# Optimization experiments

Hardware: AMD Instinct MI355X
Metric: run time of the kernel (lower is better)

## Reference

```python
import jax, jax.numpy as jnp
import numpy as np

H = 16  # n_heads
D = 64  # d_keys


def setup_inputs() -> dict:
    key = jax.random.key(0)
    ks = jax.random.split(key, 11)
    b, n, dm = 2, 2048, 1024
    s = 1.0 / np.sqrt(dm)
    return {
        "q": jax.random.normal(ks[0], (b, n, dm), jnp.float32),
        "k": jax.random.normal(ks[1], (b, n, dm), jnp.float32),
        "v": jax.random.normal(ks[2], (b, n, dm), jnp.float32),
        "Wq": jax.random.normal(ks[3], (dm, H * D), jnp.float32) * s,
        "bq": jax.random.normal(ks[4], (H * D,), jnp.float32) * 0.01,
        "Wk": jax.random.normal(ks[5], (dm, H * D), jnp.float32) * s,
        "bk": jax.random.normal(ks[6], (H * D,), jnp.float32) * 0.01,
        "Wv": jax.random.normal(ks[7], (dm, H * D), jnp.float32) * s,
        "bv": jax.random.normal(ks[8], (H * D,), jnp.float32) * 0.01,
        "Wo": jax.random.normal(ks[9], (H * D, dm), jnp.float32) * s,
        "bo": jax.random.normal(ks[10], (dm,), jnp.float32) * 0.01,
    }


def reference(q, k, v, Wq, bq, Wk, bk, Wv, bv, Wo, bo):
    b, n_q, _ = q.shape
    n_k = k.shape[1]
    # projections -> [b, n, h, d]
    qh = (q @ Wq + bq).reshape(b, n_q, H, D)
    kh = (k @ Wk + bk).reshape(b, n_k, H, D)
    vh = (v @ Wv + bv).reshape(b, n_k, H, D)
    # scores [b, h, n, m]
    scores = jnp.einsum('bnhd,bmhd->bhnm', qh, kh)
    causal = jnp.triu(jnp.ones((n_q, n_k), dtype=bool), k=1)  # True above diag
    scores = jnp.where(causal, -jnp.inf, scores)
    att = jax.nn.softmax(scores / np.sqrt(D).astype(np.float32), axis=-1)
    att_out = jnp.einsum('bhnm,bmhd->bnhd', att, vh).reshape(b, n_q, H * D)
    return att_out @ Wo + bo
```

## Files before the change

### kernel.cpp

```cpp
#include <hip/hip_runtime.h>

typedef float f32x4 __attribute__((ext_vector_type(4)));
typedef __bf16 bf16x8 __attribute__((ext_vector_type(8)));
typedef __bf16 bf16x4 __attribute__((ext_vector_type(4)));
typedef __bf16 bf16_t;

#define NH 16
#define DH 64
#define SEQ 2048
#define DM 1024

extern "C" hipError_t hipMemPtrGetInfo(void* ptr, size_t* size);

__device__ __forceinline__ bf16x8 ld8(const bf16_t* p) { return *(const bf16x8*)p; }
__device__ __forceinline__ void st8(bf16_t* p, bf16x8 v) { *(bf16x8*)p = v; }

__device__ __forceinline__ void gl_lds16(const bf16_t* g, bf16_t* l)
{
    __builtin_amdgcn_global_load_lds(
        (const __attribute__((address_space(1))) unsigned int*)g,
        (__attribute__((address_space(3))) unsigned int*)l, 16, 0, 0);
}

__global__ __launch_bounds__(256) void fill_sentinel(float* out, unsigned n, float val)
{
    unsigned stride = gridDim.x * blockDim.x;
    for (unsigned i = blockIdx.x * blockDim.x + threadIdx.x; i < n; i += stride)
        out[i] = val;
}

__global__ __launch_bounds__(256) void prep(
    const float* __restrict__ q, const float* __restrict__ k,
    const float* __restrict__ v,
    const float* __restrict__ w0, const float* __restrict__ w1,
    const float* __restrict__ w2, const float* __restrict__ w3,
    bf16_t* __restrict__ xb, bf16_t* __restrict__ wt)
{
    int z = blockIdx.z;
    if (z < 3) {
        const float* src = (z == 0) ? q : (z == 1) ? k : v;
        bf16_t* dst = xb + (size_t)z * (4096u * 1024u);
        size_t i8 = ((size_t)blockIdx.x * 256 + threadIdx.x) * 8;
        f32x4 u = *(const f32x4*)(src + i8);
        f32x4 w = *(const f32x4*)(src + i8 + 4);
        bf16x8 h = { (bf16_t)u.x, (bf16_t)u.y, (bf16_t)u.z, (bf16_t)u.w,
                     (bf16_t)w.x, (bf16_t)w.y, (bf16_t)w.z, (bf16_t)w.w };
        st8(dst + i8, h);
    } else {
        int x = blockIdx.x;
        if (x >= 1024) return;
        int w = x >> 8, rem = x & 255;
        int bx = rem & 15, by = rem >> 4;
        const float* in = (w == 0) ? w0 : (w == 1) ? w1 : (w == 2) ? w2 : w3;
        bf16_t* out = wt + (size_t)w * DM * DM;
        __shared__ __align__(16) bf16_t tile[64][72];
        int t = threadIdx.x;
        int k0 = by * 64, n0 = bx * 64;
        int r0 = t >> 4, c0 = (t & 15) * 4;
        for (int p = 0; p < 4; p++) {
            int r = r0 + p * 16;
            const float* src = in + (size_t)(k0 + r) * DM + n0 + c0;
            for (int i = 0; i < 4; i++) tile[r][c0 + i] = (bf16_t)src[i];
        }
        __syncthreads();
        for (int p = 0; p < 4; p++) {
            int rn = r0 + p * 16;
            bf16_t* dst = out + (size_t)(n0 + rn) * DM + k0 + c0;
            for (int i = 0; i < 4; i++) dst[i] = tile[c0 + i][rn];
        }
    }
}

__device__ __forceinline__ void gemm_epilogue(
    f32x4 (&acc)[4][4], const float* bias, bf16_t* out, float* outf,
    int mode, int out_is_f32, int m0, int n0, int wr0, int wc0, int g, int l16)
{
    float scale = (mode == 0) ? 0.125f : 1.0f;
    for (int mi = 0; mi < 4; mi++) {
        int mbase = m0 + wr0 + mi * 16 + g * 4;
        for (int ni = 0; ni < 4; ni++) {
            int col = n0 + wc0 + ni * 16 + l16;
            float bv = bias[col];
            if (mode == 2) {
                int bb = mbase >> 11, nn0 = mbase & 2047;
                int h = col >> 6, d = col & 63;
                bf16x4 pv;
                for (int r = 0; r < 4; r++) pv[r] = (bf16_t)(acc[mi][ni][r] + bv);
                *(bf16x4*)(out + ((size_t)(bb * NH + h) * DH + d) * SEQ + nn0) = pv;
            } else {
                for (int r = 0; r < 4; r++) {
                    int mr = mbase + r;
                    float sv = (acc[mi][ni][r] + bv) * scale;
                    if (mode == 3) {
                        if (out_is_f32) outf[(size_t)mr * 1024 + col] = sv;
                        else            out[(size_t)mr * 1024 + col] = (bf16_t)sv;
                    } else {
                        int bb = mr >> 11, nn = mr & 2047;
                        int h = col >> 6, d = col & 63;
                        out[((size_t)(bb * NH + h) * SEQ + nn) * DH + d] = (bf16_t)sv;
                    }
                }
            }
        }
    }
}

__global__ __launch_bounds__(256) void gemm_fast(
    const bf16_t* __restrict__ xb_base, const bf16_t* __restrict__ wt_base,
    const float* __restrict__ b0, const float* __restrict__ b1,
    const float* __restrict__ b2, bf16_t* __restrict__ out_base,
    float* __restrict__ outf, int mode_base, int out_is_f32)
{
    int z = blockIdx.z;
    const bf16_t* X    = xb_base + (size_t)z * (4096u * 1024u);
    const bf16_t* WT   = wt_base + (size_t)z * DM * DM;
    const float* bias  = (z == 0) ? b0 : (z == 1) ? b1 : b2;
    bf16_t* out = out_base + (size_t)z * (4096u * 1024u);
    int mode = mode_base + z;

    int m0 = blockIdx.x * 128;
    int n0 = blockIdx.y * 128;

    __shared__ __align__(16) bf16_t Alds[128 * 64];
    __shared__ __align__(16) bf16_t Blds[128 * 64];

    int t = threadIdx.x;
    int lane = t & 63, wave = t >> 6;
    int g = lane >> 4, l16 = lane & 15;
    int wr0 = (wave >> 1) * 64, wc0 = (wave & 1) * 64;
    int crow = lane >> 3;
    int ccol = (lane & 7) * 8;

    f32x4 acc[4][4] = {};

    for (int k0 = 0; k0 < DM; k0 += 64) {
        __syncthreads();
        for (int c = wave; c < 16; c += 4) {
            int row = c * 8 + crow;
            gl_lds16(X  + (size_t)(m0 + row) * DM + k0 + ccol,
                     Alds + c * 512 + lane * 8);
            gl_lds16(WT + (size_t)(n0 + row) * DM + k0 + ccol,
                     Blds + c * 512 + lane * 8);
        }
        __syncthreads();
        for (int kk = 0; kk < 2; kk++) {
            bf16x8 af[4], bfr[4];
            for (int i = 0; i < 4; i++)
                af[i] = ld8(Alds + (wr0 + i * 16 + l16) * 64 + kk * 32 + g * 8);
            for (int i = 0; i < 4; i++)
                bfr[i] = ld8(Blds + (wc0 + i * 16 + l16) * 64 + kk * 32 + g * 8);
            for (int mi = 0; mi < 4; mi++)
                for (int ni = 0; ni < 4; ni++)
                    acc[mi][ni] = __builtin_amdgcn_mfma_f32_16x16x32_bf16(
                        af[mi], bfr[ni], acc[mi][ni], 0, 0, 0);
        }
    }
    gemm_epilogue(acc, bias, out, outf, mode, out_is_f32, m0, n0, wr0, wc0, g, l16);
}

__global__ __launch_bounds__(256) void gemm_mha(
    const float* __restrict__ x0, const float* __restrict__ x1,
    const float* __restrict__ x2, const bf16_t* __restrict__ xb,
    const bf16_t* __restrict__ wt_base,
    const float* __restrict__ b0, const float* __restrict__ b1,
    const float* __restrict__ b2, bf16_t* __restrict__ out_base,
    float* __restrict__ outf, int mode_base, int out_is_f32)
{
    int z = blockIdx.z;
    const float* Xf    = (z == 0) ? x0 : (z == 1) ? x1 : x2;
    const bf16_t* WT   = wt_base + (size_t)z * DM * DM;
    const float* bias  = (z == 0) ? b0 : (z == 1) ? b1 : b2;
    bf16_t* out = out_base + (size_t)z * (4096u * 1024u);
    int mode = mode_base + z;

    int m0 = blockIdx.x * 128;
    int n0 = blockIdx.y * 128;

    __shared__ __align__(16) bf16_t Alds[128 * 64];
    __shared__ __align__(16) bf16_t Blds[128 * 64];

    int t = threadIdx.x;
    int lane = t & 63, wave = t >> 6;
    int g = lane >> 4, l16 = lane & 15;
    int wr0 = (wave >> 1) * 64, wc0 = (wave & 1) * 64;

    f32x4 acc[4][4] = {};
    int srow = t >> 3, sk = (t & 7) * 8;

    for (int k0 = 0; k0 < DM; k0 += 64) {
        __syncthreads();
        if (mode < 3) {
            for (int p = 0; p < 4; p++) {
                int r = srow + p * 32;
                const float* s4 = Xf + (size_t)(m0 + r) * DM + k0 + sk;
                f32x4 u = *(const f32x4*)s4;
                f32x4 w = *(const f32x4*)(s4 + 4);
                bf16x8 h = { (bf16_t)u.x, (bf16_t)u.y, (bf16_t)u.z, (bf16_t)u.w,
                             (bf16_t)w.x, (bf16_t)w.y, (bf16_t)w.z, (bf16_t)w.w };
                st8(Alds + r * 64 + sk, h);
            }
        } else {
            for (int p = 0; p < 4; p++) {
                int r = srow + p * 32;
                st8(Alds + r * 64 + sk, ld8(xb + (size_t)(m0 + r) * DM + k0 + sk));
            }
        }
        for (int p = 0; p < 4; p++) {
            int r = srow + p * 32;
            st8(Blds + r * 64 + sk, ld8(WT + (size_t)(n0 + r) * DM + k0 + sk));
        }
        __syncthreads();
        for (int kk = 0; kk < 2; kk++) {
            bf16x8 af[4], bfr[4];
            for (int i = 0; i < 4; i++)
                af[i] = ld8(Alds + (wr0 + i * 16 + l16) * 64 + kk * 32 + g * 8);
            for (int i = 0; i < 4; i++)
                bfr[i] = ld8(Blds + (wc0 + i * 16 + l16) * 64 + kk * 32 + g * 8);
            for (int mi = 0; mi < 4; mi++)
                for (int ni = 0; ni < 4; ni++)
                    acc[mi][ni] = __builtin_amdgcn_mfma_f32_16x16x32_bf16(
                        af[mi], bfr[ni], acc[mi][ni], 0, 0, 0);
        }
    }
    gemm_epilogue(acc, bias, out, outf, mode, out_is_f32, m0, n0, wr0, wc0, g, l16);
}

__global__ __launch_bounds__(512) void attn(
    const bf16_t* __restrict__ Qh, const bf16_t* __restrict__ Kh,
    const bf16_t* __restrict__ VT, bf16_t* __restrict__ att)
{
    int bhx = blockIdx.x;
    int yy  = blockIdx.y;
    int p   = (yy < 8) ? yy : 23 - yy;
    int TB  = 2 * p + 2;

    const bf16_t* Qb = Qh + (size_t)bhx * SEQ * DH;
    const bf16_t* Kb = Kh + (size_t)bhx * SEQ * DH;
    const bf16_t* Vb = VT + (size_t)bhx * DH * SEQ;

    __shared__ __align__(16) bf16_t Klds[2][64 * 72];
    __shared__ __align__(16) bf16_t Vlds[2][64 * 72];
    __shared__ __align__(16) bf16_t Plds[8][16 * 72];

    int t = threadIdx.x, lane = t & 63, wave = t >> 6;
    int g = lane >> 4, l16 = lane & 15;
    int srow = t >> 3, sk = (t & 7) * 8;
    int qt = 2 * p + (wave >> 2);
    int Tw = qt + 1;
    int rowl = (wave & 3) * 16 + l16;

    bf16x8 qf[2];
    for (int kk = 0; kk < 2; kk++)
        qf[kk] = ld8(Qb + (size_t)(qt * 64 + rowl) * DH + kk * 32 + g * 8);

    f32x4 accO[4] = {};
    float l = 0.f;
    bf16_t* Pw = Plds[wave];

    st8(&Klds[0][srow * 72 + sk], ld8(Kb + (size_t)srow * DH + sk));
    st8(&Vlds[0][srow * 72 + sk], ld8(Vb + (size_t)srow * SEQ + sk));

    for (int j = 0; j < TB; j++) {
        __syncthreads();
        if (j + 1 < TB) {
            int b = (j + 1) & 1;
            st8(&Klds[b][srow * 72 + sk],
                ld8(Kb + (size_t)((j + 1) * 64 + srow) * DH + sk));
            st8(&Vlds[b][srow * 72 + sk],
                ld8(Vb + (size_t)srow * SEQ + (j + 1) * 64 + sk));
        }
        if (j >= Tw) continue;
        int buf = j & 1;
        bool diag = (j == Tw - 1);

        f32x4 s[4];
        for (int c = 0; c < 4; c++) {
            f32x4 a = {};
            for (int kk = 0; kk < 2; kk++) {
                bf16x8 kf = ld8(&Klds[buf][(c * 16 + l16) * 72 + kk * 32 + g * 8]);
                a = __builtin_amdgcn_mfma_f32_16x16x32_bf16(kf, qf[kk], a, 0, 0, 0);
            }
            s[c] = a;
        }
        for (int c = 0; c < 4; c++) {
            bf16x4 pv;
            for (int r = 0; r < 4; r++) {
                float v = s[c][r];
                if (diag && (c * 16 + g * 4 + r) > rowl) v = -1e30f;
                float pe = __expf(v);
                l += pe;
                pv[r] = (bf16_t)pe;
            }
            *(bf16x4*)(Pw + l16 * 72 + c * 16 + g * 4) = pv;
        }
        asm volatile("s_waitcnt lgkmcnt(0)" ::: "memory");

        bf16x8 pf0 = ld8(Pw + l16 * 72 + g * 8);
        bf16x8 pf1 = ld8(Pw + l16 * 72 + 32 + g * 8);
        for (int c2 = 0; c2 < 4; c2++) {
            bf16x8 vf0 = ld8(&Vlds[buf][(c2 * 16 + l16) * 72 + g * 8]);
            accO[c2] = __builtin_amdgcn_mfma_f32_16x16x32_bf16(vf0, pf0, accO[c2], 0, 0, 0);
            bf16x8 vf1 = ld8(&Vlds[buf][(c2 * 16 + l16) * 72 + 32 + g * 8]);
            accO[c2] = __builtin_amdgcn_mfma_f32_16x16x32_bf16(vf1, pf1, accO[c2], 0, 0, 0);
        }

        if (diag) {
            float lt = l;
            lt += __shfl_xor(lt, 16);
            lt += __shfl_xor(lt, 32);
            float inv = 1.f / lt;
            int qabs = qt * 64 + rowl;
            int bb = bhx >> 4, h = bhx & 15;
            for (int c2 = 0; c2 < 4; c2++) {
                bf16x4 ov;
                for (int r = 0; r < 4; r++) ov[r] = (bf16_t)(accO[c2][r] * inv);
                *(bf16x4*)(att + (((size_t)bb * SEQ + qabs) * NH + h) * DH
                           + c2 * 16 + g * 4) = ov;
            }
        }
    }
}

extern "C" void kernel_launch(void* const* d_in, const int* in_sizes, int n_in,
                              void* d_out, int out_size, void* d_ws, size_t ws_size,
                              hipStream_t stream) {
    const float* q  = (const float*)d_in[0];
    const float* k  = (const float*)d_in[1];
    const float* v  = (const float*)d_in[2];
    const float* Wq = (const float*)d_in[3];
    const float* bq = (const float*)d_in[4];
    const float* Wk = (const float*)d_in[5];
    const float* bk = (const float*)d_in[6];
    const float* Wv = (const float*)d_in[7];
    const float* bv = (const float*)d_in[8];
    const float* Wo = (const float*)d_in[9];
    const float* bo = (const float*)d_in[10];

    const size_t MAT = 1024u * 1024u;
    const size_t BIG = 4096u * 1024u;
    const size_t NEED_BASE = 64 + (4 * BIG + 4 * MAT) * 2;
    const size_t NEED_FAST = NEED_BASE + 3 * BIG * 2;

    if (ws_size < NEED_BASE) {
        fill_sentinel<<<1024, 256, 0, stream>>>((float*)d_out,
                                                (unsigned)out_size, 100.0f);
        return;
    }

    int out_is_f32 = 1;
    size_t osz = 0;
    if (hipMemPtrGetInfo(d_out, &osz) == hipSuccess && osz != 0 &&
        osz < (size_t)out_size * 4)
        out_is_f32 = 0;

    bf16_t* base = (bf16_t*)d_ws + 32;
    bf16_t* Qh  = base;
    bf16_t* Kh  = Qh + BIG;
    bf16_t* VT  = Kh + BIG;
    bf16_t* att = VT + BIG;
    bf16_t* WT  = att + BIG;
    bf16_t* Xb  = WT + 4 * MAT;

    if (ws_size >= NEED_FAST) {
        prep<<<dim3(2048, 1, 4), 256, 0, stream>>>(q, k, v, Wq, Wk, Wv, Wo, Xb, WT);
        gemm_fast<<<dim3(32, 8, 3), 256, 0, stream>>>(Xb, WT, bq, bk, bv,
                                                      Qh, nullptr, 0, 0);
        attn<<<dim3(32, 16), 512, 0, stream>>>(Qh, Kh, VT, att);
        gemm_fast<<<dim3(32, 8, 1), 256, 0, stream>>>(att, WT + 3 * MAT,
                                                      bo, bo, bo,
                                                      (bf16_t*)d_out, (float*)d_out,
                                                      3, out_is_f32);
    } else {
        prep<<<dim3(2048, 1, 4), 256, 0, stream>>>(q, k, v, Wq, Wk, Wv, Wo,
                                                   (bf16_t*)d_ws, WT);
        gemm_mha<<<dim3(32, 8, 3), 256, 0, stream>>>(q, k, v, nullptr, WT,
                                                     bq, bk, bv, Qh, nullptr, 0, 0);
        attn<<<dim3(32, 16), 512, 0, stream>>>(Qh, Kh, VT, att);
        gemm_mha<<<dim3(32, 8, 1), 256, 0, stream>>>(nullptr, nullptr, nullptr, att,
                                                     WT + 3 * MAT, bo, bo, bo,
                                                     (bf16_t*)d_out, (float*)d_out,
                                                     3, out_is_f32);
    }
}
```

Baseline: 245.7 us.

## Add 256x256-tile double-buffered QKV projection GEMM with 512 threads

Replaces the 128x128-tile QKV projection GEMM with a new kernel that uses 256x256 tiles, 8 waves per block, and double-buffered LDS staging via direct global-to-LDS loads with an XOR swizzle. The larger tile raises arithmetic intensity per loaded byte, and the double buffering overlaps loads with MFMA work. The grid shrinks to 192 blocks, which may underfill the GPU's compute units. The 128 KB of LDS per block also limits occupancy. The V output is written transposed with 4-wide vector stores.

```diff
diff --git a/kernel.cpp b/kernel.cpp
--- a/kernel.cpp
+++ b/kernel.cpp
@@ -105,6 +105,114 @@
     }
 }
 
+__global__ __launch_bounds__(512, 2) void gemm_qkv(
+    const bf16_t* __restrict__ xb_base, const bf16_t* __restrict__ wt_base,
+    const float* __restrict__ b0, const float* __restrict__ b1,
+    const float* __restrict__ b2, bf16_t* __restrict__ out_base)
+{
+    int z = blockIdx.z;
+    const bf16_t* X  = xb_base + (size_t)z * (4096u * 1024u);
+    const bf16_t* WT = wt_base + (size_t)z * DM * DM;
+    const float* bias = (z == 0) ? b0 : (z == 1) ? b1 : b2;
+    bf16_t* out = out_base + (size_t)z * (4096u * 1024u);
+
+    int m0 = blockIdx.x * 256;
+    int n0 = blockIdx.y * 256;
+
+    __shared__ __align__(16) bf16_t Ab[2][256 * 64];
+    __shared__ __align__(16) bf16_t Bb[2][256 * 64];
+
+    int tid  = threadIdx.x;
+    int lane = tid & 63, w = tid >> 6;
+    int g = lane >> 4, l16 = lane & 15;
+    int wr0 = (w >> 2) * 128;
+    int wc0 = (w & 3) * 64;
+    int rl = lane >> 3, cl = lane & 7;
+
+    f32x4 acc[8][4] = {};
+
+    auto stage = [&](int b, int t) {
+        int k0 = t * 64;
+        #pragma unroll
+        for (int i = 0; i < 4; i++) {
+            int row = i * 64 + w * 8 + rl;
+            int cs  = cl ^ (row & 7);
+            gl_lds16(X + (size_t)(m0 + row) * DM + k0 + cs * 8,
+                     &Ab[b][(i * 64 + w * 8) * 64 + lane * 8]);
+        }
+        #pragma unroll
+        for (int i = 0; i < 4; i++) {
+            int row = i * 64 + w * 8 + rl;
+            int cs  = cl ^ (row & 7);
+            gl_lds16(WT + (size_t)(n0 + row) * DM + k0 + cs * 8,
+                     &Bb[b][(i * 64 + w * 8) * 64 + lane * 8]);
+        }
+    };
+
+    stage(0, 0);
+    stage(1, 1);
+    __syncthreads();
+
+    for (int t = 0; t < 16; t++) {
+        int b = t & 1;
+        bf16x8 bfr[4][2];
+        #pragma unroll
+        for (int ni = 0; ni < 4; ni++) {
+            int rn = wc0 + ni * 16 + l16;
+            #pragma unroll
+            for (int kk = 0; kk < 2; kk++)
+                bfr[ni][kk] = ld8(&Bb[b][rn * 64 + (((kk * 4 + g) ^ (rn & 7)) * 8)]);
+        }
+        #pragma unroll
+        for (int mp = 0; mp < 4; mp++) {
+            bf16x8 af[2][2];
+            #pragma unroll
+            for (int i = 0; i < 2; i++) {
+                int ra = wr0 + (mp * 2 + i) * 16 + l16;
+                #pragma unroll
+                for (int kk = 0; kk < 2; kk++)
+                    af[i][kk] = ld8(&Ab[b][ra * 64 + (((kk * 4 + g) ^ (ra & 7)) * 8)]);
+            }
+            __builtin_amdgcn_s_setprio(1);
+            #pragma unroll
+            for (int i = 0; i < 2; i++)
+                #pragma unroll
+                for (int ni = 0; ni < 4; ni++)
+                    #pragma unroll
+                    for (int kk = 0; kk < 2; kk++)
+                        acc[mp * 2 + i][ni] = __builtin_amdgcn_mfma_f32_16x16x32_bf16(
+                            af[i][kk], bfr[ni][kk], acc[mp * 2 + i][ni], 0, 0, 0);
+            __builtin_amdgcn_s_setprio(0);
+        }
+        __syncthreads();
+        if (t + 2 < 16) stage(b, t + 2);
+    }
+
+    float scale = (z == 0) ? 0.125f : 1.0f;
+    #pragma unroll
+    for (int mi = 0; mi < 8; mi++) {
+        int mbase = m0 + wr0 + mi * 16 + g * 4;
+        int bb = mbase >> 11, nn0 = mbase & 2047;
+        #pragma unroll
+        for (int ni = 0; ni < 4; ni++) {
+            int col = n0 + wc0 + ni * 16 + l16;
+            float bv = bias[col];
+            int h = col >> 6, d = col & 63;
+            if (z == 2) {
+                bf16x4 pv;
+                for (int r = 0; r < 4; r++) pv[r] = (bf16_t)(acc[mi][ni][r] + bv);
+                *(bf16x4*)(out + ((size_t)(bb * NH + h) * DH + d) * SEQ + nn0) = pv;
+            } else {
+                for (int r = 0; r < 4; r++) {
+                    int nn = nn0 + r;
+                    out[((size_t)(bb * NH + h) * SEQ + nn) * DH + d] =
+                        (bf16_t)((acc[mi][ni][r] + bv) * scale);
+                }
+            }
+        }
+    }
+}
+
 __global__ __launch_bounds__(256) void gemm_fast(
     const bf16_t* __restrict__ xb_base, const bf16_t* __restrict__ wt_base,
     const float* __restrict__ b0, const float* __restrict__ b1,
@@ -363,8 +471,7 @@
 
     if (ws_size >= NEED_FAST) {
         prep<<<dim3(2048, 1, 4), 256, 0, stream>>>(q, k, v, Wq, Wk, Wv, Wo, Xb, WT);
-        gemm_fast<<<dim3(32, 8, 3), 256, 0, stream>>>(Xb, WT, bq, bk, bv,
-                                                      Qh, nullptr, 0, 0);
+        gemm_qkv<<<dim3(16, 4, 3), 512, 0, stream>>>(Xb, WT, bq, bk, bv, Qh);
         attn<<<dim3(32, 16), 512, 0, stream>>>(Qh, Kh, VT, att);
         gemm_fast<<<dim3(32, 8, 1), 256, 0, stream>>>(att, WT + 3 * MAT,
                                                       bo, bo, bo,
```

Result: faster. 234.2 us (-4.7%).

## Add 256x256-tile pipelined QKV projection GEMM with quadrant-interleaved LDS double buffering

Applied to the files above, without the earlier changes.

Replaces the 128x128-tile QKV projection GEMM with a new 512-thread kernel that computes 256x256 output tiles as four 128x128 quadrants. Global-to-LDS loads for the next k-step are interleaved with MFMA work on the current quadrants, using explicit waitcnt, barriers and setprio so that memory traffic overlaps compute. It also writes V directly in transposed layout with vector stores. The larger tiles increase operand reuse but launch only 192 blocks, fewer than the 256 CUs, and the hand-scheduled waitcnt ordering is fragile.

```diff
diff --git a/kernel.cpp b/kernel.cpp
--- a/kernel.cpp
+++ b/kernel.cpp
@@ -105,6 +105,124 @@
     }
 }
 
+#define LGKM0 asm volatile("s_waitcnt lgkmcnt(0)" ::: "memory")
+#define VMC(n) asm volatile("s_waitcnt vmcnt(" #n ")" ::: "memory")
+#define BARRIER __builtin_amdgcn_s_barrier()
+
+#define STA(d, h, dk) do { \
+    _Pragma("unroll") for (int j = 0; j < 2; j++) \
+        gl_lds16(Xp + ((h) * 128 + j * 64) * DM + (dk) * 64, \
+                 Ab + sdst0 + ((d) * 2 + (h)) * 8192 + j * 4096); } while (0)
+#define STB(d, h, dk) do { \
+    _Pragma("unroll") for (int j = 0; j < 2; j++) \
+        gl_lds16(Wp + ((h) * 128 + j * 64) * DM + (dk) * 64, \
+                 Bb + sdst0 + ((d) * 2 + (h)) * 8192 + j * 4096); } while (0)
+#define RDA(d, h, F) do { \
+    _Pragma("unroll") for (int mf = 0; mf < 4; mf++) { \
+        F[mf][0] = ld8(Ab + rA0 + ((d) * 2 + (h)) * 8192 + mf * 1024); \
+        F[mf][1] = ld8(Ab + rA1 + ((d) * 2 + (h)) * 8192 + mf * 1024); } } while (0)
+#define RDB(d, h, F) do { \
+    _Pragma("unroll") for (int nf = 0; nf < 2; nf++) { \
+        F[nf][0] = ld8(Bb + rB0 + ((d) * 2 + (h)) * 8192 + nf * 1024); \
+        F[nf][1] = ld8(Bb + rB1 + ((d) * 2 + (h)) * 8192 + nf * 1024); } } while (0)
+#define MMQ(AF, BF, Q) do { \
+    __builtin_amdgcn_s_setprio(1); \
+    _Pragma("unroll") for (int mf = 0; mf < 4; mf++) \
+        _Pragma("unroll") for (int nf = 0; nf < 2; nf++) { \
+            Q[mf][nf] = __builtin_amdgcn_mfma_f32_16x16x32_bf16( \
+                AF[mf][0], BF[nf][0], Q[mf][nf], 0, 0, 0); \
+            Q[mf][nf] = __builtin_amdgcn_mfma_f32_16x16x32_bf16( \
+                AF[mf][1], BF[nf][1], Q[mf][nf], 0, 0, 0); } \
+    __builtin_amdgcn_s_setprio(0); } while (0)
+
+__global__ __launch_bounds__(512, 2) void gemm_qkv(
+    const bf16_t* __restrict__ xb_base, const bf16_t* __restrict__ wt_base,
+    const float* __restrict__ b0v, const float* __restrict__ b1v,
+    const float* __restrict__ b2v, bf16_t* __restrict__ out_base)
+{
+    int z = blockIdx.z;
+    const bf16_t* X  = xb_base + (size_t)z * (4096u * 1024u);
+    const bf16_t* WT = wt_base + (size_t)z * DM * DM;
+    const float* bias = (z == 0) ? b0v : (z == 1) ? b1v : b2v;
+    bf16_t* out = out_base + (size_t)z * (4096u * 1024u);
+
+    int m0 = blockIdx.x * 256;
+    int n0 = blockIdx.y * 256;
+
+    __shared__ __align__(16) bf16_t Ab[2 * 2 * 128 * 64];
+    __shared__ __align__(16) bf16_t Bb[2 * 2 * 128 * 64];
+
+    int tid  = threadIdx.x;
+    int lane = tid & 63, w = tid >> 6;
+    int g = lane >> 4, l16 = lane & 15;
+    int wm = w >> 2, wn = w & 3;
+    int rl = lane >> 3, cl = lane & 7;
+    int w8 = w * 8;
+
+    int srow = w8 + rl;
+    int scol = (cl ^ rl) * 8;
+    const bf16_t* Xp = X  + (size_t)(m0 + srow) * DM + scol;
+    const bf16_t* Wp = WT + (size_t)(n0 + srow) * DM + scol;
+    int sdst0 = w8 * 64 + lane * 8;
+
+    int x7 = l16 & 7;
+    int rA0 = (wm * 64 + l16) * 64 + ((0 + g) ^ x7) * 8;
+    int rA1 = (wm * 64 + l16) * 64 + ((4 + g) ^ x7) * 8;
+    int rB0 = (wn * 32 + l16) * 64 + ((0 + g) ^ x7) * 8;
+    int rB1 = (wn * 32 + l16) * 64 + ((4 + g) ^ x7) * 8;
+
+    f32x4 a00[4][2] = {}, a01[4][2] = {}, a10[4][2] = {}, a11[4][2] = {};
+    bf16x8 afA[4][2], afB[4][2], bA[2][2], bB[2][2];
+
+    STA(0, 0, 0); STB(0, 0, 0); STA(0, 1, 0); STB(0, 1, 0);
+    STA(1, 0, 1); STB(1, 0, 1); STA(1, 1, 1);
+    VMC(6);
+    BARRIER;
+    RDA(0, 0, afA); RDB(0, 0, bA);
+
+    #pragma unroll 1
+    for (int i = 0; i < 7; i++) {
+        STB(1, 1, 1); LGKM0; RDB(0, 1, bB); MMQ(afA, bA, a00); BARRIER;
+        STA(0, 0, 2); LGKM0; RDA(0, 1, afB); MMQ(afA, bB, a01); BARRIER;
+        STB(0, 0, 2); VMC(4); LGKM0; MMQ(afB, bA, a10); BARRIER;
+        STA(0, 1, 2); RDA(1, 0, afA); RDB(1, 0, bA); MMQ(afB, bB, a11); BARRIER;
+        STB(0, 1, 2); LGKM0; RDB(1, 1, bB); MMQ(afA, bA, a00); BARRIER;
+        STA(1, 0, 3); LGKM0; RDA(1, 1, afB); MMQ(afA, bB, a01); BARRIER;
+        STB(1, 0, 3); VMC(4); LGKM0; MMQ(afB, bA, a10); BARRIER;
+        STA(1, 1, 3); RDA(0, 0, afA); RDB(0, 0, bA); MMQ(afB, bB, a11); BARRIER;
+        Xp += 128; Wp += 128;
+    }
+    STB(1, 1, 1); LGKM0; RDB(0, 1, bB); MMQ(afA, bA, a00); BARRIER;
+    LGKM0; RDA(0, 1, afB); MMQ(afA, bB, a01); BARRIER;
+    VMC(0); LGKM0; MMQ(afB, bA, a10); BARRIER;
+    RDA(1, 0, afA); RDB(1, 0, bA); MMQ(afB, bB, a11); BARRIER;
+    LGKM0; RDB(1, 1, bB); MMQ(afA, bA, a00); BARRIER;
+    LGKM0; RDA(1, 1, afB); MMQ(afA, bB, a01); BARRIER;
+    LGKM0; MMQ(afB, bA, a10); BARRIER;
+    MMQ(afB, bB, a11);
+
+    float scale = (z == 0) ? 0.125f : 1.0f;
+#define EPI(Q, Mh, Nh) do { \
+    _Pragma("unroll") for (int mf = 0; mf < 4; mf++) { \
+        int mbase = m0 + (Mh) * 128 + wm * 64 + mf * 16 + g * 4; \
+        int bb = mbase >> 11, nn0 = mbase & 2047; \
+        _Pragma("unroll") for (int nf = 0; nf < 2; nf++) { \
+            int col = n0 + (Nh) * 128 + wn * 32 + nf * 16 + l16; \
+            float bv = bias[col]; \
+            int hh = col >> 6, dd = col & 63; \
+            if (z == 2) { \
+                bf16x4 pv; \
+                for (int r = 0; r < 4; r++) pv[r] = (bf16_t)(Q[mf][nf][r] + bv); \
+                *(bf16x4*)(out + ((size_t)(bb * NH + hh) * DH + dd) * SEQ + nn0) = pv; \
+            } else { \
+                for (int r = 0; r < 4; r++) \
+                    out[((size_t)(bb * NH + hh) * SEQ + nn0 + r) * DH + dd] = \
+                        (bf16_t)((Q[mf][nf][r] + bv) * scale); \
+            } } } } while (0)
+    EPI(a00, 0, 0); EPI(a01, 0, 1); EPI(a10, 1, 0); EPI(a11, 1, 1);
+#undef EPI
+}
+
 __global__ __launch_bounds__(256) void gemm_fast(
     const bf16_t* __restrict__ xb_base, const bf16_t* __restrict__ wt_base,
     const float* __restrict__ b0, const float* __restrict__ b1,
@@ -363,8 +481,7 @@
 
     if (ws_size >= NEED_FAST) {
         prep<<<dim3(2048, 1, 4), 256, 0, stream>>>(q, k, v, Wq, Wk, Wv, Wo, Xb, WT);
-        gemm_fast<<<dim3(32, 8, 3), 256, 0, stream>>>(Xb, WT, bq, bk, bv,
-                                                      Qh, nullptr, 0, 0);
+        gemm_qkv<<<dim3(16, 4, 3), 512, 0, stream>>>(Xb, WT, bq, bk, bv, Qh);
         attn<<<dim3(32, 16), 512, 0, stream>>>(Qh, Kh, VT, att);
         gemm_fast<<<dim3(32, 8, 1), 256, 0, stream>>>(att, WT + 3 * MAT,
                                                       bo, bo, bo,
```

New measurement: 225.5 us. 8.2% less time.
